# Performance work log

Measured on AMD Instinct MI355X. Metric: run time of the kernel, lower is better.

The kernel has to match this reference:

```python
import jax, jax.numpy as jnp
import numpy as np

W = 192      # image width (seq len for attn1)
HN = 192     # H * N (seq len for attn2)
C = 128      # hidden_dim
NHEAD = 8


def setup_inputs() -> dict:
    key = jax.random.key(0)
    ks = jax.random.split(key, 12)
    sc = 0.05  # small init so softmax is well-conditioned
    feat = jax.random.normal(ks[0], (W, 2 * HN, C), jnp.float32)
    pos = jax.random.normal(ks[1], (2 * W - 1, C), jnp.float32)
    pos_y = jax.random.normal(ks[2], (2 * HN - 1, C), jnp.float32)
    i = jnp.arange(W)
    pos_indexes = (i[:, None] - i[None, :] + W - 1).reshape(-1).astype(jnp.int32)
    j = jnp.arange(HN)
    pos_indexes_y = (j[:, None] - j[None, :] + HN - 1).reshape(-1).astype(jnp.int32)
    return {
        "feat": feat,
        "pos": pos,
        "pos_y": pos_y,
        "ln_w": jnp.ones((C,), jnp.float32),
        "ln_b": jnp.zeros((C,), jnp.float32),
        "w_in1": jax.random.normal(ks[3], (3 * C, C), jnp.float32) * sc,
        "b_in1": jnp.zeros((3 * C,), jnp.float32),
        "w_out1": jax.random.normal(ks[4], (C, C), jnp.float32) * sc,
        "b_out1": jnp.zeros((C,), jnp.float32),
        "w_in2": jax.random.normal(ks[5], (3 * C, C), jnp.float32) * sc,
        "b_in2": jnp.zeros((3 * C,), jnp.float32),
        "w_out2": jax.random.normal(ks[6], (C, C), jnp.float32) * sc,
        "b_out2": jnp.zeros((C,), jnp.float32),
        "pos_indexes": pos_indexes,
        "pos_indexes_y": pos_indexes_y,
    }


def _layernorm(x, g, b, eps=1e-5):
    m = x.mean(-1, keepdims=True)
    v = ((x - m) ** 2).mean(-1, keepdims=True)
    return (x - m) / jnp.sqrt(v + eps) * g + b


def _rel_attn(x, pos_enc, pos_idx, w_in, b_in, w_out, b_out):
    # x: [w, bsz, c]; pos_enc: [2w-1, c]; pos_idx: [w*w]
    w, bsz, c = x.shape
    hd = c // NHEAD
    scale = float(hd) ** -0.5
    q, k, v = jnp.split(x @ w_in.T + b_in, 3, axis=-1)
    pe = pos_enc[pos_idx].reshape(w, w, c)           # [w, w, c] relative pos
    q_r, k_r = jnp.split(pe @ w_in[: 2 * c].T + b_in[: 2 * c], 2, axis=-1)
    q = (q * scale).reshape(w, bsz, NHEAD, hd)
    k = k.reshape(w, bsz, NHEAD, hd)
    v = v.reshape(w, bsz, NHEAD, hd)
    q_r = (q_r * scale).reshape(w, w, NHEAD, hd)
    k_r = k_r.reshape(w, w, NHEAD, hd)
    # content-content + content-pos + pos-content -> [bsz, nhead, w, w]
    attn = (jnp.einsum('wnec,vnec->newv', q, k)
            + jnp.einsum('wnec,wvec->newv', q, k_r)
            + jnp.einsum('vnec,wvec->newv', k, q_r))
    attn = jax.nn.softmax(attn, axis=-1)
    out = jnp.einsum('newv,vnec->wnec', attn, v).reshape(w, bsz, c)
    return out @ w_out.T + b_out


def reference(feat, pos, pos_y, ln_w, ln_b,
              w_in1, b_in1, w_out1, b_out1,
              w_in2, b_in2, w_out2, b_out2,
              pos_indexes, pos_indexes_y):
    w, h2, c = feat.shape
    f2 = _layernorm(feat, ln_w, ln_b)
    # [W, 2HN, C] -> [HN, 2W, C]: attention along vertical (H) axis
    f2 = f2.reshape(w, 2, h2 // 2, c).transpose(2, 1, 0, 3).reshape(h2 // 2, 2 * w, c)
    f2 = _rel_attn(f2, pos_y, pos_indexes_y, w_in2, b_in2, w_out2, b_out2)
    # back to [W, 2HN, C]: attention along horizontal (W) axis
    f2 = f2.reshape(h2 // 2, 2, w, c).transpose(2, 1, 0, 3).reshape(w, h2, c)
    f2 = _rel_attn(f2, pos, pos_indexes, w_in1, b_in1, w_out1, b_out1)
    return feat + f2
```

## Files before the change

### kernel.cpp

```cpp
#include <hip/hip_runtime.h>
#include <hip/hip_bf16.h>


typedef unsigned short u16;
typedef short bf16x4 __attribute__((ext_vector_type(4)));
typedef short bf16x8 __attribute__((ext_vector_type(8)));
typedef float f32x4 __attribute__((ext_vector_type(4)));
typedef float f32x16 __attribute__((ext_vector_type(16)));

__device__ inline u16 f2bf(float f) {
    union { float f; unsigned u; } a; a.f = f;
    unsigned u = a.u;
    unsigned r = u + 0x7FFFu + ((u >> 16) & 1u);
    return (u16)(r >> 16);
}
__device__ inline float bf2f(u16 x) {
    union { unsigned u; float f; } a; a.u = ((unsigned)x) << 16;
    return a.f;
}

__global__ __launch_bounds__(256) void ln_kernel(const float* __restrict__ feat,
                                                 const float* __restrict__ g,
                                                 const float* __restrict__ bta,
                                                 u16* __restrict__ x2) {
    int wid = threadIdx.x >> 6, lane = threadIdx.x & 63;
    int r = blockIdx.x * 4 + wid;
    const float* row = feat + (size_t)r * 128;
    float v0 = row[lane], v1 = row[lane + 64];
    float s = v0 + v1;
    for (int m = 1; m < 64; m <<= 1) s += __shfl_xor(s, m);
    float mean = s * (1.0f / 128.0f);
    float d0 = v0 - mean, d1 = v1 - mean;
    float vs = d0 * d0 + d1 * d1;
    for (int m = 1; m < 64; m <<= 1) vs += __shfl_xor(vs, m);
    float rstd = rsqrtf(vs * (1.0f / 128.0f) + 1e-5f);
    int w = r / 384, rem = r % 384;
    int out_r = (rem % 192) * 384 + (rem / 192) * 192 + w;
    u16* orow = x2 + (size_t)out_r * 128;
    orow[lane]      = f2bf(d0 * rstd * g[lane] + bta[lane]);
    orow[lane + 64] = f2bf(d1 * rstd * g[lane + 64] + bta[lane + 64]);
}

__global__ __launch_bounds__(256) void posproj_kernel(const float* __restrict__ pos,
                                                      const float* __restrict__ w_in,
                                                      const float* __restrict__ b_in,
                                                      u16* __restrict__ qr,
                                                      u16* __restrict__ kr) {
    int d = blockIdx.x, t = threadIdx.x;
    if (d == 383) {
        if (t < 128)      { int e = t >> 4,  j = t & 15;  qr[(e * 384 + 383) * 16 + j] = 0; }
        else              { int t2 = t - 128; int e = t2 >> 4, j = t2 & 15; kr[(e * 384 + 383) * 16 + j] = 0; }
        return;
    }
    __shared__ float prow[128];
    if (t < 128) prow[t] = pos[d * 128 + t];
    __syncthreads();
    const float* wrow = w_in + t * 128;
    float acc = b_in[t];
    #pragma unroll 8
    for (int k = 0; k < 128; ++k) acc += prow[k] * wrow[k];
    int which = t >> 7, e = (t >> 4) & 7, j = t & 15;
    if (which == 0) qr[(e * 384 + d) * 16 + j] = f2bf(acc * 0.25f);
    else            kr[(e * 384 + d) * 16 + j] = f2bf(acc);
}

__global__ __launch_bounds__(256) void qkv_gemm(const u16* __restrict__ X,
                                                const float* __restrict__ Wn,
                                                const float* __restrict__ bias,
                                                u16* __restrict__ Qo,
                                                u16* __restrict__ Ko,
                                                u16* __restrict__ Vo) {
    __shared__ u16 a_lds[128][136];
    __shared__ u16 w_lds[64][136];
    int tid = threadIdx.x;
    int m0 = blockIdx.y * 128, n0 = blockIdx.x * 64;
    #pragma unroll
    for (int i = 0; i < 8; ++i) {
        int idx = tid + 256 * i;
        int row = idx >> 4, c8 = (idx & 15) * 8;
        *(int4*)&a_lds[row][c8] = *(const int4*)&X[(size_t)(m0 + row) * 128 + c8];
    }
    #pragma unroll
    for (int i = 0; i < 8; ++i) {
        int idx = tid + 256 * i;
        int row = idx >> 5, c4 = (idx & 31) * 4;
        float4 f = *(const float4*)&Wn[(size_t)(n0 + row) * 128 + c4];
        uint2 p;
        p.x = (unsigned)f2bf(f.x) | ((unsigned)f2bf(f.y) << 16);
        p.y = (unsigned)f2bf(f.z) | ((unsigned)f2bf(f.w) << 16);
        *(uint2*)&w_lds[row][c4] = p;
    }
    __syncthreads();
    int lane = tid & 63, wid = tid >> 6;
    int wr = (wid >> 1) * 64, wc = (wid & 1) * 32;
    int kg = lane >> 4, l15 = lane & 15;
    f32x4 acc[4][2];
    #pragma unroll
    for (int i = 0; i < 4; ++i)
        #pragma unroll
        for (int j = 0; j < 2; ++j) acc[i][j] = (f32x4){0.f, 0.f, 0.f, 0.f};
    #pragma unroll
    for (int kk = 0; kk < 4; ++kk) {
        int kof = kk * 32 + kg * 8;
        bf16x8 a[4], b[2];
        #pragma unroll
        for (int i = 0; i < 4; ++i) a[i] = *(const bf16x8*)&a_lds[wr + i * 16 + l15][kof];
        #pragma unroll
        for (int j = 0; j < 2; ++j) b[j] = *(const bf16x8*)&w_lds[wc + j * 16 + l15][kof];
        #pragma unroll
        for (int i = 0; i < 4; ++i)
            #pragma unroll
            for (int j = 0; j < 2; ++j)
                acc[i][j] = __builtin_amdgcn_mfma_f32_16x16x32_bf16(a[i], b[j], acc[i][j], 0, 0, 0);
    }
    #pragma unroll
    for (int i = 0; i < 4; ++i)
        #pragma unroll
        for (int j = 0; j < 2; ++j) {
            int col_g = n0 + wc + j * 16 + l15;
            float bv = bias[col_g];
            int which = col_g >> 7, e = (col_g >> 4) & 7, d = col_g & 15;
            u16* dst = which == 0 ? Qo : (which == 1 ? Ko : Vo);
            float scl = which == 0 ? 0.25f : 1.0f;
            #pragma unroll
            for (int ii = 0; ii < 4; ++ii) {
                int row_g = m0 + wr + i * 16 + kg * 4 + ii;
                int batch = row_g % 384, sq = row_g / 384;
                dst[((size_t)(batch * 8 + e) * 192 + sq) * 16 + d] = f2bf((acc[i][j][ii] + bv) * scl);
            }
        }
}

__global__ __launch_bounds__(512, 4) void attn_kernel(const u16* __restrict__ Qg,
                                                      const u16* __restrict__ Kg,
                                                      const u16* __restrict__ Vg,
                                                      const u16* __restrict__ qr_g,
                                                      const u16* __restrict__ kr_g,
                                                      u16* __restrict__ Og) {
    __shared__ float sc[96][194];
    __shared__ u16 Vt[16][200];
    int tid = threadIdx.x, lane = tid & 63, wid = tid >> 6;
    int half = blockIdx.x, e = blockIdx.y, b = blockIdx.z;
    int w0 = half * 96;
    size_t base = ((size_t)b * 8 + e) * 192 * 16;

    #pragma unroll
    for (int i = 0; i < 6; ++i) { int idx = tid + 512 * i;
        Vt[idx & 15][idx >> 4] = Vg[base + idx]; }

    int lo = lane & 31, hi = lane >> 5, hi8 = hi * 8;
    const u16* Qrow  = Qg + base;
    const u16* Krow  = Kg + base;
    const u16* krrow = kr_g + (size_t)e * 384 * 16;
    const u16* qrrow = qr_g + (size_t)e * 384 * 16;

    #pragma unroll
    for (int it = 0; it < 3; ++it) {
        int t = wid + 8 * it;
        if (t < 18) {
            int wt = t / 6, vt = t % 6;
            bf16x8 a  = *(const bf16x8*)(Qrow + (size_t)(w0 + wt * 32 + lo) * 16 + hi8);
            bf16x8 bb = *(const bf16x8*)(Krow + (size_t)(vt * 32 + lo) * 16 + hi8);
            f32x16 acc = {};
            acc = __builtin_amdgcn_mfma_f32_32x32x16_bf16(a, bb, acc, 0, 0, 0);
            #pragma unroll
            for (int ii = 0; ii < 16; ++ii) {
                int row = wt * 32 + (ii & 3) + 8 * (ii >> 2) + 4 * hi;
                sc[row][vt * 32 + lo] = acc[ii];
            }
        }
    }
    __syncthreads();

    #pragma unroll
    for (int it = 0; it < 3; ++it) {
        int t = wid + 8 * it;
        if (t < 21) {
            int wt = t / 7, dj = t % 7;
            int d0 = w0 + wt * 32 + dj * 32;
            bf16x8 a  = *(const bf16x8*)(Qrow + (size_t)(w0 + wt * 32 + lo) * 16 + hi8);
            bf16x8 bb = *(const bf16x8*)(krrow + (size_t)(d0 + lo) * 16 + hi8);
            f32x16 acc = {};
            acc = __builtin_amdgcn_mfma_f32_32x32x16_bf16(a, bb, acc, 0, 0, 0);
            int vbase = w0 + wt * 32 + 191 - d0 - lo + 4 * hi;
            int wlb = wt * 32 + 4 * hi;
            #pragma unroll
            for (int ii = 0; ii < 16; ++ii) {
                int rr = (ii & 3) + 8 * (ii >> 2);
                int v = vbase + rr;
                int col = ((unsigned)v < 192u) ? v : 192;
                sc[wlb + rr][col] += acc[ii];
            }
        }
    }
    __syncthreads();

    #pragma unroll
    for (int it = 0; it < 3; ++it) {
        int t = wid + 8 * it;
        if (t < 24) {
            int vt = t >> 2, dj = t & 3;
            int V0 = vt * 32;
            int d0 = w0 + 160 - V0 + dj * 32;
            bf16x8 a  = *(const bf16x8*)(qrrow + (size_t)(d0 + lo) * 16 + hi8);
            bf16x8 bb = *(const bf16x8*)(Krow + (size_t)(V0 + lo) * 16 + hi8);
            f32x16 acc = {};
            acc = __builtin_amdgcn_mfma_f32_32x32x16_bf16(a, bb, acc, 0, 0, 0);
            int v = V0 + lo;
            int wlb = d0 + 4 * hi + v - 191 - w0;
            #pragma unroll
            for (int ii = 0; ii < 16; ++ii) {
                int rr = (ii & 3) + 8 * (ii >> 2);
                int wl = wlb + rr;
                float* p = ((unsigned)wl < 96u) ? &sc[wl][v] : &sc[0][192];
                *p += acc[ii];
            }
        }
    }
    __syncthreads();

    #pragma unroll
    for (int p = 0; p < 3; ++p) {
        int r = wid * 12 + p * 4 + (lane >> 4);
        int j = lane & 15;
        float x[12];
        #pragma unroll
        for (int k = 0; k < 6; ++k)
            *(float2*)&x[k * 2] = *(const float2*)&sc[r][j * 12 + k * 2];
        float sum = 0.f;
        #pragma unroll
        for (int k = 0; k < 12; ++k) { x[k] = __expf(x[k]); sum += x[k]; }
        unsigned* prow32 = (unsigned*)&sc[r][0];
        #pragma unroll
        for (int k = 0; k < 6; ++k)
            prow32[j * 6 + k] = (unsigned)f2bf(x[2 * k]) | ((unsigned)f2bf(x[2 * k + 1]) << 16);
        sum += __shfl_xor(sum, 1);
        sum += __shfl_xor(sum, 2);
        sum += __shfl_xor(sum, 4);
        sum += __shfl_xor(sum, 8);
        if (j == 0) sc[r][193] = 1.0f / sum;
    }
    __syncthreads();

    if (wid < 6) {
        int l15 = lane & 15, kg = lane >> 4;
        const u16* prow = (const u16*)&sc[wid * 16 + l15][0];
        f32x4 acc = (f32x4){0.f, 0.f, 0.f, 0.f};
        #pragma unroll
        for (int kt = 0; kt < 6; ++kt) {
            bf16x4 a0 = *(const bf16x4*)(prow + kt * 32 + kg * 8);
            bf16x4 a1 = *(const bf16x4*)(prow + kt * 32 + kg * 8 + 4);
            bf16x8 a;
            a[0] = a0[0]; a[1] = a0[1]; a[2] = a0[2]; a[3] = a0[3];
            a[4] = a1[0]; a[5] = a1[1]; a[6] = a1[2]; a[7] = a1[3];
            bf16x8 bb = *(const bf16x8*)&Vt[l15][kt * 32 + kg * 8];
            acc = __builtin_amdgcn_mfma_f32_16x16x32_bf16(a, bb, acc, 0, 0, 0);
        }
        #pragma unroll
        for (int ii = 0; ii < 4; ++ii) {
            int wl = wid * 16 + kg * 4 + ii;
            float val = acc[ii] * sc[wl][193];
            Og[((size_t)(w0 + wl) * 384 + b) * 128 + e * 16 + l15] = f2bf(val);
        }
    }
}

template <int MODE>
__global__ __launch_bounds__(256) void outproj_gemm(const u16* __restrict__ X,
                                                    const float* __restrict__ Wn,
                                                    const float* __restrict__ bias,
                                                    const float* __restrict__ feat,
                                                    u16* __restrict__ x1o,
                                                    float* __restrict__ outp) {
    __shared__ u16 a_lds[128][136];
    __shared__ u16 w_lds[64][136];
    int tid = threadIdx.x;
    int m0 = blockIdx.y * 128, n0 = blockIdx.x * 64;
    #pragma unroll
    for (int i = 0; i < 8; ++i) {
        int idx = tid + 256 * i;
        int row = idx >> 4, c8 = (idx & 15) * 8;
        *(int4*)&a_lds[row][c8] = *(const int4*)&X[(size_t)(m0 + row) * 128 + c8];
    }
    #pragma unroll
    for (int i = 0; i < 8; ++i) {
        int idx = tid + 256 * i;
        int row = idx >> 5, c4 = (idx & 31) * 4;
        float4 f = *(const float4*)&Wn[(size_t)(n0 + row) * 128 + c4];
        uint2 p;
        p.x = (unsigned)f2bf(f.x) | ((unsigned)f2bf(f.y) << 16);
        p.y = (unsigned)f2bf(f.z) | ((unsigned)f2bf(f.w) << 16);
        *(uint2*)&w_lds[row][c4] = p;
    }
    __syncthreads();
    int lane = tid & 63, wid = tid >> 6;
    int wr = (wid >> 1) * 64, wc = (wid & 1) * 32;
    int kg = lane >> 4, l15 = lane & 15;
    f32x4 acc[4][2];
    #pragma unroll
    for (int i = 0; i < 4; ++i)
        #pragma unroll
        for (int j = 0; j < 2; ++j) acc[i][j] = (f32x4){0.f, 0.f, 0.f, 0.f};
    #pragma unroll
    for (int kk = 0; kk < 4; ++kk) {
        int kof = kk * 32 + kg * 8;
        bf16x8 a[4], b[2];
        #pragma unroll
        for (int i = 0; i < 4; ++i) a[i] = *(const bf16x8*)&a_lds[wr + i * 16 + l15][kof];
        #pragma unroll
        for (int j = 0; j < 2; ++j) b[j] = *(const bf16x8*)&w_lds[wc + j * 16 + l15][kof];
        #pragma unroll
        for (int i = 0; i < 4; ++i)
            #pragma unroll
            for (int j = 0; j < 2; ++j)
                acc[i][j] = __builtin_amdgcn_mfma_f32_16x16x32_bf16(a[i], b[j], acc[i][j], 0, 0, 0);
    }
    #pragma unroll
    for (int i = 0; i < 4; ++i)
        #pragma unroll
        for (int j = 0; j < 2; ++j) {
            int col_g = n0 + wc + j * 16 + l15;
            float bv = bias[col_g];
            #pragma unroll
            for (int ii = 0; ii < 4; ++ii) {
                int row_g = m0 + wr + i * 16 + kg * 4 + ii;
                float val = acc[i][j][ii] + bv;
                if (MODE == 0) {
                    int h = row_g / 384, rem = row_g % 384, s2 = rem / 192, w = rem % 192;
                    x1o[((size_t)(w * 384 + s2 * 192 + h)) * 128 + col_g] = f2bf(val);
                } else {
                    size_t o = (size_t)row_g * 128 + col_g;
                    outp[o] = val + feat[o];
                }
            }
        }
}

extern "C" void kernel_launch(void* const* d_in, const int* in_sizes, int n_in,
                              void* d_out, int out_size, void* d_ws, size_t ws_size,
                              hipStream_t stream) {
    const float* feat   = (const float*)d_in[0];
    const float* pos    = (const float*)d_in[1];
    const float* pos_y  = (const float*)d_in[2];
    const float* ln_w   = (const float*)d_in[3];
    const float* ln_b   = (const float*)d_in[4];
    const float* w_in1  = (const float*)d_in[5];
    const float* b_in1  = (const float*)d_in[6];
    const float* w_out1 = (const float*)d_in[7];
    const float* b_out1 = (const float*)d_in[8];
    const float* w_in2  = (const float*)d_in[9];
    const float* b_in2  = (const float*)d_in[10];
    const float* w_out2 = (const float*)d_in[11];
    const float* b_out2 = (const float*)d_in[12];
    float* out = (float*)d_out;

    char* ws = (char*)d_ws;
    const size_t R = (size_t)73728 * 128;
    u16* x2 = (u16*)ws; ws += R * 2;
    u16* x1 = (u16*)ws; ws += R * 2;
    u16* Q  = (u16*)ws; ws += R * 2;
    u16* K  = (u16*)ws; ws += R * 2;
    u16* V  = (u16*)ws; ws += R * 2;
    u16* O  = (u16*)ws; ws += R * 2;
    u16* qr = (u16*)ws; ws += (size_t)8 * 384 * 16 * 2;
    u16* kr = (u16*)ws; ws += (size_t)8 * 384 * 16 * 2;

    ln_kernel<<<18432, 256, 0, stream>>>(feat, ln_w, ln_b, x2);
    posproj_kernel<<<384, 256, 0, stream>>>(pos_y, w_in2, b_in2, qr, kr);
    qkv_gemm<<<dim3(6, 576), 256, 0, stream>>>(x2, w_in2, b_in2, Q, K, V);
    attn_kernel<<<dim3(2, 8, 384), 512, 0, stream>>>(Q, K, V, qr, kr, O);
    outproj_gemm<0><<<dim3(2, 576), 256, 0, stream>>>(O, w_out2, b_out2, nullptr, x1, nullptr);
    posproj_kernel<<<384, 256, 0, stream>>>(pos, w_in1, b_in1, qr, kr);
    qkv_gemm<<<dim3(6, 576), 256, 0, stream>>>(x1, w_in1, b_in1, Q, K, V);
    attn_kernel<<<dim3(2, 8, 384), 512, 0, stream>>>(Q, K, V, qr, kr, O);
    outproj_gemm<1><<<dim3(2, 576), 256, 0, stream>>>(O, w_out1, b_out1, feat, nullptr, out);
}
```

Measured before the change: 363.6 us.

## Swap MFMA operands in attention to vectorize LDS score writes and specialize tiles

The attention kernel now swaps the A/B operands of the score MFMAs so each lane holds contiguous columns, letting the content-content tile be written with 128-bit LDS stores. The relative-position tiles are split into full tiles with no bounds checks and partial tiles that keep the clamped path. The score row stride is padded to 196 so rows stay 16-byte aligned for vector reads. Softmax now uses the hardware packed bf16 convert and wider LDS loads and stores, and the PV stage reads 8 bf16 values per load. The aim is fewer LDS instructions and less index arithmetic, at the cost of possible new bank conflicts and rounding that differs from the software bf16 conversion.

```diff
diff --git a/kernel.cpp b/kernel.cpp
--- a/kernel.cpp
+++ b/kernel.cpp
@@ -3,7 +3,6 @@
 
 
 typedef unsigned short u16;
-typedef short bf16x4 __attribute__((ext_vector_type(4)));
 typedef short bf16x8 __attribute__((ext_vector_type(8)));
 typedef float f32x4 __attribute__((ext_vector_type(4)));
 typedef float f32x16 __attribute__((ext_vector_type(16)));
@@ -14,9 +13,10 @@
     unsigned r = u + 0x7FFFu + ((u >> 16) & 1u);
     return (u16)(r >> 16);
 }
-__device__ inline float bf2f(u16 x) {
-    union { unsigned u; float f; } a; a.u = ((unsigned)x) << 16;
-    return a.f;
+__device__ inline unsigned cvt_pk_bf16(float lo, float hi) {
+    unsigned r;
+    asm("v_cvt_pk_bf16_f32 %0, %1, %2" : "=v"(r) : "v"(lo), "v"(hi));
+    return r;
 }
 
 __global__ __launch_bounds__(256) void ln_kernel(const float* __restrict__ feat,
@@ -137,7 +137,7 @@
                                                       const u16* __restrict__ qr_g,
                                                       const u16* __restrict__ kr_g,
                                                       u16* __restrict__ Og) {
-    __shared__ float sc[96][194];
+    __shared__ float sc[96][196];
     __shared__ u16 Vt[16][200];
     int tid = threadIdx.x, lane = tid & 63, wid = tid >> 6;
     int half = blockIdx.x, e = blockIdx.y, b = blockIdx.z;
@@ -153,20 +153,22 @@
     const u16* Krow  = Kg + base;
     const u16* krrow = kr_g + (size_t)e * 384 * 16;
     const u16* qrrow = qr_g + (size_t)e * 384 * 16;
+    float* scf = &sc[0][0];
 
     #pragma unroll
     for (int it = 0; it < 3; ++it) {
         int t = wid + 8 * it;
         if (t < 18) {
             int wt = t / 6, vt = t % 6;
-            bf16x8 a  = *(const bf16x8*)(Qrow + (size_t)(w0 + wt * 32 + lo) * 16 + hi8);
-            bf16x8 bb = *(const bf16x8*)(Krow + (size_t)(vt * 32 + lo) * 16 + hi8);
+            bf16x8 ak = *(const bf16x8*)(Krow + (size_t)(vt * 32 + lo) * 16 + hi8);
+            bf16x8 bq = *(const bf16x8*)(Qrow + (size_t)(w0 + wt * 32 + lo) * 16 + hi8);
             f32x16 acc = {};
-            acc = __builtin_amdgcn_mfma_f32_32x32x16_bf16(a, bb, acc, 0, 0, 0);
+            acc = __builtin_amdgcn_mfma_f32_32x32x16_bf16(ak, bq, acc, 0, 0, 0);
+            float* dst = &sc[wt * 32 + lo][vt * 32 + 4 * hi];
             #pragma unroll
-            for (int ii = 0; ii < 16; ++ii) {
-                int row = wt * 32 + (ii & 3) + 8 * (ii >> 2) + 4 * hi;
-                sc[row][vt * 32 + lo] = acc[ii];
+            for (int g = 0; g < 4; ++g) {
+                f32x4 vv = { acc[4 * g], acc[4 * g + 1], acc[4 * g + 2], acc[4 * g + 3] };
+                *(f32x4*)(dst + 8 * g) = vv;
             }
         }
     }
@@ -176,20 +178,32 @@
     for (int it = 0; it < 3; ++it) {
         int t = wid + 8 * it;
         if (t < 21) {
-            int wt = t / 7, dj = t % 7;
+            int wt, dj, partial;
+            if (t < 6) { wt = t >> 1; dj = (t & 1) * 6; partial = 1; }
+            else       { int u = t - 6; wt = u / 5; dj = u % 5 + 1; partial = 0; }
             int d0 = w0 + wt * 32 + dj * 32;
-            bf16x8 a  = *(const bf16x8*)(Qrow + (size_t)(w0 + wt * 32 + lo) * 16 + hi8);
-            bf16x8 bb = *(const bf16x8*)(krrow + (size_t)(d0 + lo) * 16 + hi8);
+            bf16x8 akr = *(const bf16x8*)(krrow + (size_t)(d0 + lo) * 16 + hi8);
+            bf16x8 bq  = *(const bf16x8*)(Qrow + (size_t)(w0 + wt * 32 + lo) * 16 + hi8);
             f32x16 acc = {};
-            acc = __builtin_amdgcn_mfma_f32_32x32x16_bf16(a, bb, acc, 0, 0, 0);
-            int vbase = w0 + wt * 32 + 191 - d0 - lo + 4 * hi;
-            int wlb = wt * 32 + 4 * hi;
-            #pragma unroll
-            for (int ii = 0; ii < 16; ++ii) {
-                int rr = (ii & 3) + 8 * (ii >> 2);
-                int v = vbase + rr;
-                int col = ((unsigned)v < 192u) ? v : 192;
-                sc[wlb + rr][col] += acc[ii];
+            acc = __builtin_amdgcn_mfma_f32_32x32x16_bf16(akr, bq, acc, 0, 0, 0);
+            int wl = wt * 32 + lo;
+            int vC = lo + 191 - 32 * dj - 4 * hi;
+            if (!partial) {
+                float* pf = scf + wl * 196 + (vC - 27);
+                #pragma unroll
+                for (int ii = 0; ii < 16; ++ii) {
+                    const int rr = (ii & 3) + 8 * (ii >> 2);
+                    pf[27 - rr] += acc[ii];
+                }
+            } else {
+                float* rowp = scf + wl * 196;
+                #pragma unroll
+                for (int ii = 0; ii < 16; ++ii) {
+                    const int rr = (ii & 3) + 8 * (ii >> 2);
+                    int v = vC - rr;
+                    int col = ((unsigned)v < 192u) ? v : 192;
+                    rowp[col] += acc[ii];
+                }
             }
         }
     }
@@ -199,21 +213,32 @@
     for (int it = 0; it < 3; ++it) {
         int t = wid + 8 * it;
         if (t < 24) {
-            int vt = t >> 2, dj = t & 3;
+            int vt, dj, partial;
+            if (t < 12) { vt = t >> 1; dj = (t & 1) * 3; partial = 1; }
+            else        { int u = t - 12; vt = u >> 1; dj = (u & 1) + 1; partial = 0; }
             int V0 = vt * 32;
             int d0 = w0 + 160 - V0 + dj * 32;
-            bf16x8 a  = *(const bf16x8*)(qrrow + (size_t)(d0 + lo) * 16 + hi8);
-            bf16x8 bb = *(const bf16x8*)(Krow + (size_t)(V0 + lo) * 16 + hi8);
+            bf16x8 aqr = *(const bf16x8*)(qrrow + (size_t)(d0 + lo) * 16 + hi8);
+            bf16x8 bk  = *(const bf16x8*)(Krow + (size_t)(V0 + lo) * 16 + hi8);
             f32x16 acc = {};
-            acc = __builtin_amdgcn_mfma_f32_32x32x16_bf16(a, bb, acc, 0, 0, 0);
-            int v = V0 + lo;
-            int wlb = d0 + 4 * hi + v - 191 - w0;
-            #pragma unroll
-            for (int ii = 0; ii < 16; ++ii) {
-                int rr = (ii & 3) + 8 * (ii >> 2);
-                int wl = wlb + rr;
-                float* p = ((unsigned)wl < 96u) ? &sc[wl][v] : &sc[0][192];
-                *p += acc[ii];
+            acc = __builtin_amdgcn_mfma_f32_32x32x16_bf16(aqr, bk, acc, 0, 0, 0);
+            int wlB = 32 * dj - 31 + 4 * hi + lo;
+            if (!partial) {
+                float* pf = scf + wlB * 196 + V0 + lo;
+                #pragma unroll
+                for (int ii = 0; ii < 16; ++ii) {
+                    const int rr = (ii & 3) + 8 * (ii >> 2);
+                    pf[rr * 196] += acc[ii];
+                }
+            } else {
+                #pragma unroll
+                for (int ii = 0; ii < 16; ++ii) {
+                    const int rr = (ii & 3) + 8 * (ii >> 2);
+                    int wl = wlB + rr;
+                    float* p = ((unsigned)wl < 96u) ? (scf + wl * 196 + V0 + lo)
+                                                    : (scf + 192);
+                    *p += acc[ii];
+                }
             }
         }
     }
@@ -223,17 +248,22 @@
     for (int p = 0; p < 3; ++p) {
         int r = wid * 12 + p * 4 + (lane >> 4);
         int j = lane & 15;
-        float x[12];
-        #pragma unroll
-        for (int k = 0; k < 6; ++k)
-            *(float2*)&x[k * 2] = *(const float2*)&sc[r][j * 12 + k * 2];
+        f32x4 x0 = *(const f32x4*)&sc[r][j * 12];
+        f32x4 x1 = *(const f32x4*)&sc[r][j * 12 + 4];
+        f32x4 x2 = *(const f32x4*)&sc[r][j * 12 + 8];
+        float xs[12];
+        #pragma unroll
+        for (int k = 0; k < 4; ++k) { xs[k] = __expf(x0[k]); xs[4 + k] = __expf(x1[k]); xs[8 + k] = __expf(x2[k]); }
         float sum = 0.f;
         #pragma unroll
-        for (int k = 0; k < 12; ++k) { x[k] = __expf(x[k]); sum += x[k]; }
+        for (int k = 0; k < 12; ++k) sum += xs[k];
+        unsigned pk[6];
+        #pragma unroll
+        for (int k = 0; k < 6; ++k) pk[k] = cvt_pk_bf16(xs[2 * k], xs[2 * k + 1]);
         unsigned* prow32 = (unsigned*)&sc[r][0];
-        #pragma unroll
-        for (int k = 0; k < 6; ++k)
-            prow32[j * 6 + k] = (unsigned)f2bf(x[2 * k]) | ((unsigned)f2bf(x[2 * k + 1]) << 16);
+        *(uint2*)&prow32[j * 6]     = *(uint2*)&pk[0];
+        *(uint2*)&prow32[j * 6 + 2] = *(uint2*)&pk[2];
+        *(uint2*)&prow32[j * 6 + 4] = *(uint2*)&pk[4];
         sum += __shfl_xor(sum, 1);
         sum += __shfl_xor(sum, 2);
         sum += __shfl_xor(sum, 4);
@@ -248,11 +278,7 @@
         f32x4 acc = (f32x4){0.f, 0.f, 0.f, 0.f};
         #pragma unroll
         for (int kt = 0; kt < 6; ++kt) {
-            bf16x4 a0 = *(const bf16x4*)(prow + kt * 32 + kg * 8);
-            bf16x4 a1 = *(const bf16x4*)(prow + kt * 32 + kg * 8 + 4);
-            bf16x8 a;
-            a[0] = a0[0]; a[1] = a0[1]; a[2] = a0[2]; a[3] = a0[3];
-            a[4] = a1[0]; a[5] = a1[1]; a[6] = a1[2]; a[7] = a1[3];
+            bf16x8 a  = *(const bf16x8*)(prow + kt * 32 + kg * 8);
             bf16x8 bb = *(const bf16x8*)&Vt[l15][kt * 32 + kg * 8];
             acc = __builtin_amdgcn_mfma_f32_16x16x32_bf16(a, bb, acc, 0, 0, 0);
         }
```

After: 356.5 us. Within noise of the previous version (-2.0%).
